# Kernel tuning notes

Measured on AMD Instinct MI355X. Metric: run time of the kernel, lower is better.

The kernel has to match this reference:

```python
import jax, jax.numpy as jnp
import numpy as np

B, S, E, H = 4, 2048, 1024, 16
D = E // H  # head_dim = 64
SCALE = D ** -0.5
NEG_INF = -1e9


def setup_inputs() -> dict:
    key = jax.random.key(0)
    ks = jax.random.split(key, 12)
    p = 1.0 / np.sqrt(E)  # nn.Linear default init scale
    inp = {
        'query': jax.random.normal(ks[0], (B, S, E), jnp.float32),
        'key': jax.random.normal(ks[1], (B, S, E), jnp.float32),
        'value': jax.random.normal(ks[2], (B, S, E), jnp.float32),
        'mask': jnp.ones((B, S, S), jnp.int32),
        'Wq': jax.random.uniform(ks[3], (E, E), jnp.float32, -p, p),
        'bq': jax.random.uniform(ks[4], (E,), jnp.float32, -p, p),
        'Wk': jax.random.uniform(ks[5], (E, E), jnp.float32, -p, p),
        'bk': jax.random.uniform(ks[6], (E,), jnp.float32, -p, p),
        'Wv': jax.random.uniform(ks[7], (E, E), jnp.float32, -p, p),
        'bv': jax.random.uniform(ks[8], (E,), jnp.float32, -p, p),
        'Wo': jax.random.uniform(ks[9], (E, E), jnp.float32, -p, p),
        'bo': jax.random.uniform(ks[10], (E,), jnp.float32, -p, p),
    }
    return inp


def _heads(x):
    # [B, S, E] -> [B, H, S, D]
    b, s, _ = x.shape
    return x.reshape(b, s, H, D).transpose(0, 2, 1, 3)


def reference(query, key, value, mask, Wq, bq, Wk, bk, Wv, bv, Wo, bo):
    # separate QKV projections (nn.Linear: x @ W.T + b)
    q = _heads(query @ Wq.T + bq) * SCALE  # query pre-scaled as in module
    k = _heads(key @ Wk.T + bk)
    v = _heads(value @ Wv.T + bv)
    # scaled dot-product attention with explicit score matrix
    scores = jnp.einsum('bhqd,bhkd->bhqk', q, k)  # [B, H, S, S]
    m = mask[:, None, :, :]  # broadcast over heads
    scores = jnp.where(m == 0, NEG_INF, scores)
    attn = jax.nn.softmax(scores, axis=-1)
    out = jnp.einsum('bhqk,bhkd->bhqd', attn, v)  # [B, H, S, D]
    out = out.transpose(0, 2, 1, 3).reshape(query.shape[0], -1, E)
    return out @ Wo.T + bo
```

## Files before the change

### kernel.cpp

```cpp
#include <hip/hip_runtime.h>


#define B_ 4
#define S_ 2048
#define E_ 1024
#define H_ 16
#define D_ 64

typedef __attribute__((ext_vector_type(4))) float f32x4;
typedef __attribute__((ext_vector_type(8))) short short8;
typedef __attribute__((ext_vector_type(4))) short short4v;
typedef __attribute__((ext_vector_type(8))) __bf16 bf16x8;
typedef __attribute__((ext_vector_type(4))) __bf16 bf16x4;
typedef unsigned short u16;
typedef unsigned int u32;

#define MFMA16(A, Bf, C) __builtin_amdgcn_mfma_f32_16x16x32_bf16((A), (Bf), (C), 0, 0, 0)

#define FMAXB2 12.0f

__device__ __forceinline__ f32x4 mfma_pv(short4v a, short4v b, f32x4 c) {
  return __builtin_amdgcn_mfma_f32_16x16x16bf16_1k(a, b, c, 0, 0, 0);
}

__device__ __forceinline__ u16 f2bf(float f) {
  u32 u = __float_as_uint(f);
  u += 0x7FFFu + ((u >> 16) & 1u);
  return (u16)(u >> 16);
}

__device__ __forceinline__ void async16(const void* g, void* l) {
  __builtin_amdgcn_global_load_lds((const __attribute__((address_space(1))) u32*)g,
                                   (__attribute__((address_space(3))) u32*)l, 16, 0, 0);
}

__device__ __forceinline__ short4v packp(float a, float b, float c, float d) {
  bf16x4 t;
  t[0] = (__bf16)a; t[1] = (__bf16)b; t[2] = (__bf16)c; t[3] = (__bf16)d;
  return __builtin_bit_cast(short4v, t);
}

__device__ __forceinline__ float exp2fast(float x) {
  return __builtin_amdgcn_exp2f(x);
}

__global__ __launch_bounds__(256) void cvt7_kernel(const float* __restrict__ a0,
                                                   const float* __restrict__ a1,
                                                   const float* __restrict__ a2,
                                                   const float* __restrict__ w0,
                                                   const float* __restrict__ w1,
                                                   const float* __restrict__ w2,
                                                   const float* __restrict__ w3,
                                                   u16* __restrict__ da0,
                                                   u16* __restrict__ da1,
                                                   u16* __restrict__ da2,
                                                   u16* __restrict__ dw0,
                                                   u16* __restrict__ dw1,
                                                   u16* __restrict__ dw2,
                                                   u16* __restrict__ dw3,
                                                   int n4a, int n4w) {
  int z = blockIdx.y;
  const float* src;
  u16* dst;
  int n4;
  switch (z) {
    case 0: src = a0; dst = da0; n4 = n4a; break;
    case 1: src = a1; dst = da1; n4 = n4a; break;
    case 2: src = a2; dst = da2; n4 = n4a; break;
    case 3: src = w0; dst = dw0; n4 = n4w; break;
    case 4: src = w1; dst = dw1; n4 = n4w; break;
    case 5: src = w2; dst = dw2; n4 = n4w; break;
    default: src = w3; dst = dw3; n4 = n4w; break;
  }
  int i = blockIdx.x * 256 + threadIdx.x;
  if (i >= n4) return;
  float4 v = ((const float4*)src)[i];
  short4v o;
  o[0] = (short)f2bf(v.x); o[1] = (short)f2bf(v.y);
  o[2] = (short)f2bf(v.z); o[3] = (short)f2bf(v.w);
  ((short4v*)dst)[i] = o;
}

__global__ __launch_bounds__(64) void mask_pack_kernel(const int* __restrict__ mask,
                                                       u32* __restrict__ mbits,
                                                       int* __restrict__ rowOK) {
  int row = blockIdx.x;
  int t = threadIdx.x;
  const int4* p = (const int4*)(mask + (size_t)row * S_ + t * 32);
  u32 bits = 0;
#pragma unroll
  for (int i = 0; i < 8; ++i) {
    int4 v = p[i];
    bits |= (v.x != 0 ? 1u : 0u) << (i * 4 + 0);
    bits |= (v.y != 0 ? 1u : 0u) << (i * 4 + 1);
    bits |= (v.z != 0 ? 1u : 0u) << (i * 4 + 2);
    bits |= (v.w != 0 ? 1u : 0u) << (i * 4 + 3);
  }
  mbits[(size_t)row * 64 + t] = bits;
  unsigned long long all1 = __ballot(bits == 0xFFFFFFFFu);
  if (t == 0) rowOK[row] = (all1 == 0xFFFFFFFFFFFFFFFFull) ? 1 : 0;
}

__device__ __forceinline__ void gemm_swizzle(int* m0, int* n0) {
  int s = blockIdx.y * 8 + blockIdx.x;
  int L = (s & 7) * 64 + (s >> 3);
  *m0 = (L >> 3) * 128;
  *n0 = (L & 7) * 128;
}

__device__ __forceinline__ void gemm_mainloop_128(const u16* __restrict__ A,
                                                  const u16* __restrict__ W,
                                                  int m0, int n0,
                                                  u16* As, u16* Bs,
                                                  f32x4 acc[4][4], int tid) {
  int w = tid >> 6, l = tid & 63, lo = l & 15, g = l >> 4;
  int wm = w >> 1, wn = w & 1;
  int srow = w * 32 + (l >> 3);
  int scol = ((l & 7) ^ (l >> 3)) * 8;
  const u16* ga0 = A + (size_t)(m0 + srow) * E_ + scol;
  const u16* gb0 = W + (size_t)(n0 + srow) * E_ + scol;
  char* la0 = (char*)As + w * 4096;
  char* lb0 = (char*)Bs + w * 4096;

  for (int k0 = 0; k0 < E_; k0 += 64) {
#pragma unroll
    for (int i = 0; i < 4; ++i) {
      async16(ga0 + (size_t)i * 8 * E_ + k0, la0 + i * 1024);
      async16(gb0 + (size_t)i * 8 * E_ + k0, lb0 + i * 1024);
    }
    __syncthreads();
#pragma unroll
    for (int kh = 0; kh < 2; ++kh) {
      bf16x8 af[4], bf[4];
#pragma unroll
      for (int mi = 0; mi < 4; ++mi) {
        int r = wm * 64 + mi * 16 + lo;
        af[mi] = *(const bf16x8*)((char*)As + r * 128 + (((kh * 4 + g) ^ (r & 7)) * 16));
      }
#pragma unroll
      for (int ni = 0; ni < 4; ++ni) {
        int r = wn * 64 + ni * 16 + lo;
        bf[ni] = *(const bf16x8*)((char*)Bs + r * 128 + (((kh * 4 + g) ^ (r & 7)) * 16));
      }
#pragma unroll
      for (int mi = 0; mi < 4; ++mi)
#pragma unroll
        for (int ni = 0; ni < 4; ++ni)
          acc[mi][ni] = MFMA16(af[mi], bf[ni], acc[mi][ni]);
    }
    __syncthreads();
  }
}

__global__ __launch_bounds__(256) void gemm_qkv_kernel(
    const u16* __restrict__ qin, const u16* __restrict__ kin, const u16* __restrict__ vin,
    const u16* __restrict__ wq, const u16* __restrict__ wk, const u16* __restrict__ wv,
    const float* __restrict__ bq, const float* __restrict__ bk, const float* __restrict__ bv,
    u16* __restrict__ Qo, u16* __restrict__ Ko, u16* __restrict__ Vo) {
  __shared__ u16 As[128 * 64];
  __shared__ u16 Bs[128 * 64];
  int z = blockIdx.z;
  const u16* A = z == 0 ? qin : (z == 1 ? kin : vin);
  const u16* W = z == 0 ? wq : (z == 1 ? wk : wv);
  const float* bias = z == 0 ? bq : (z == 1 ? bk : bv);
  u16* O = z == 0 ? Qo : (z == 1 ? Ko : Vo);
  float scale = z == 0 ? 0.125f * 1.44269504f : 1.0f;
  int m0, n0;
  gemm_swizzle(&m0, &n0);
  f32x4 acc[4][4];
#pragma unroll
  for (int mi = 0; mi < 4; ++mi)
#pragma unroll
    for (int ni = 0; ni < 4; ++ni) acc[mi][ni] = (f32x4){0.f, 0.f, 0.f, 0.f};
  int tid = threadIdx.x;
  gemm_mainloop_128(A, W, m0, n0, As, Bs, acc, tid);
  int w = tid >> 6, l = tid & 63, lo = l & 15, g = l >> 4;
  int wm = w >> 1, wn = w & 1;
#pragma unroll
  for (int mi = 0; mi < 4; ++mi)
#pragma unroll
    for (int ni = 0; ni < 4; ++ni) {
      int n = n0 + wn * 64 + ni * 16 + lo;
      int h = n >> 6, d = n & 63;
      float bb = bias[n];
      int mbase = m0 + wm * 64 + mi * 16 + g * 4;
      int b = mbase >> 11, s = mbase & 2047;
      if (z == 2) {
        short4v ov;
#pragma unroll
        for (int j = 0; j < 4; ++j) ov[j] = (short)f2bf(acc[mi][ni][j] + bb);
        *(short4v*)(O + (((size_t)(b * H_ + h)) * D_ + d) * S_ + s) = ov;
      } else {
#pragma unroll
        for (int j = 0; j < 4; ++j) {
          float val = (acc[mi][ni][j] + bb) * scale;
          O[(((size_t)(b * H_ + h)) * S_ + (s + j)) * D_ + d] = f2bf(val);
        }
      }
    }
}

__global__ __launch_bounds__(256) void gemm_out_kernel(const u16* __restrict__ A,
                                                       const u16* __restrict__ W,
                                                       const float* __restrict__ bias,
                                                       float* __restrict__ O) {
  __shared__ u16 As[128 * 64];
  __shared__ u16 Bs[128 * 64];
  int m0, n0;
  gemm_swizzle(&m0, &n0);
  f32x4 acc[4][4];
#pragma unroll
  for (int mi = 0; mi < 4; ++mi)
#pragma unroll
    for (int ni = 0; ni < 4; ++ni) acc[mi][ni] = (f32x4){0.f, 0.f, 0.f, 0.f};
  int tid = threadIdx.x;
  gemm_mainloop_128(A, W, m0, n0, As, Bs, acc, tid);
  int w = tid >> 6, l = tid & 63, lo = l & 15, g = l >> 4;
  int wm = w >> 1, wn = w & 1;
#pragma unroll
  for (int mi = 0; mi < 4; ++mi)
#pragma unroll
    for (int ni = 0; ni < 4; ++ni) {
      int n = n0 + wn * 64 + ni * 16 + lo;
      float bb = bias[n];
#pragma unroll
      for (int j = 0; j < 4; ++j) {
        int m = m0 + wm * 64 + mi * 16 + g * 4 + j;
        O[(size_t)m * E_ + n] = acc[mi][ni][j] + bb;
      }
    }
}

__global__ __launch_bounds__(256) void attn_kernel(const u16* __restrict__ Q,
                                                   const u16* __restrict__ K,
                                                   const u16* __restrict__ VT,
                                                   u16* __restrict__ AO,
                                                   const u32* __restrict__ mbits,
                                                   const int* __restrict__ rowOK) {
  __shared__ u16 Kt0[4096], Kt1[4096];
  __shared__ u16 Vt0[4096], Vt1[4096];
  __shared__ int s_ok;

  int tid = threadIdx.x;
  int w = tid >> 6, l = tid & 63, lo = l & 15, g = l >> 4;
  int flat = blockIdx.y * gridDim.x + blockIdx.x;
  int L = (flat & 7) * 128 + (flat >> 3);
  int bh = L >> 4;
  int b = bh >> 4, h = bh & 15;
  int q0 = (L & 15) * 128;

  if (tid == 0) s_ok = 1;
  __syncthreads();
  if (tid < 128 && rowOK[b * S_ + q0 + tid] == 0) s_ok = 0;
  __syncthreads();
  const bool use_mask = (s_ok == 0);

  const u16* Qb = Q + (size_t)bh * S_ * D_;
  const u16* Kb = K + (size_t)bh * S_ * D_;
  const u16* VTb = VT + (size_t)bh * D_ * S_;

  const u16* kg[2];
  const u16* vgb[2];
  int lbase[2];
#pragma unroll
  for (int r = 0; r < 2; ++r) {
    int kb = r * 4 + w;
    int tr = kb * 8 + (l >> 3);
    int dc = (l & 7) ^ (l >> 3);
    kg[r] = Kb + (size_t)tr * D_ + dc * 8;
    vgb[r] = VTb + (size_t)tr * S_ + dc * 8;
    lbase[r] = kb * 512;
  }
#pragma unroll
  for (int r = 0; r < 2; ++r) {
    async16(kg[r], &Kt0[lbase[r]]);
    async16(vgb[r], &Vt0[lbase[r]]);
  }

  int qrow = q0 + w * 32;
  bf16x8 qf[2][2];
#pragma unroll
  for (int qi = 0; qi < 2; ++qi)
#pragma unroll
    for (int kc = 0; kc < 2; ++kc)
      qf[qi][kc] = *(const bf16x8*)(Qb + (size_t)(qrow + qi * 16 + lo) * D_ + kc * 32 + g * 8);

  f32x4 ot[4][2];
  f32x4 lacc[2];
#pragma unroll
  for (int di = 0; di < 4; ++di)
#pragma unroll
    for (int qi = 0; qi < 2; ++qi) ot[di][qi] = (f32x4){0.f, 0.f, 0.f, 0.f};
  lacc[0] = (f32x4){0.f, 0.f, 0.f, 0.f};
  lacc[1] = (f32x4){0.f, 0.f, 0.f, 0.f};
  float m_run[2] = {-__builtin_inff(), -__builtin_inff()};
  const short4v onesv = {(short)0x3F80, (short)0x3F80, (short)0x3F80, (short)0x3F80};
  const f32x4 cinit = {-FMAXB2, -FMAXB2, -FMAXB2, -FMAXB2};

  auto tile_body = [&](const u16* KtC, const u16* VtC, u16* KtN, u16* VtN, int kk) {
    __syncthreads();
    if (kk + 64 < S_) {
#pragma unroll
      for (int r = 0; r < 2; ++r) {
        async16(kg[r] + (size_t)(kk + 64) * D_, &KtN[lbase[r]]);
        async16(vgb[r] + (kk + 64), &VtN[lbase[r]]);
      }
    }
    const char* Ktc = (const char*)KtC;
    const char* Vtc = (const char*)VtC;

    short4v pb[4][2];
    if (!use_mask) {
      __builtin_amdgcn_s_setprio(1);
#pragma unroll
      for (int ks = 0; ks < 4; ++ks) {
        int row = ks * 16 + lo;
        bf16x8 a0 = *(const bf16x8*)(Ktc + row * 128 + ((g * 16) ^ ((row & 7) << 4)));
        bf16x8 a1 = *(const bf16x8*)(Ktc + row * 128 + ((64 + g * 16) ^ ((row & 7) << 4)));
        f32x4 c0 = MFMA16(a0, qf[0][0], cinit);
        c0 = MFMA16(a1, qf[0][1], c0);
        f32x4 c1 = MFMA16(a0, qf[1][0], cinit);
        c1 = MFMA16(a1, qf[1][1], c1);
        pb[ks][0] = packp(exp2fast(c0[0]), exp2fast(c0[1]), exp2fast(c0[2]),
                          exp2fast(c0[3]));
        pb[ks][1] = packp(exp2fast(c1[0]), exp2fast(c1[1]), exp2fast(c1[2]),
                          exp2fast(c1[3]));
      }
      __builtin_amdgcn_s_setprio(0);
    } else {
      float tmx[2] = {-__builtin_inff(), -__builtin_inff()};
#pragma unroll
      for (int ks = 0; ks < 4; ++ks) {
        int row = ks * 16 + lo;
        bf16x8 a0 = *(const bf16x8*)(Ktc + row * 128 + ((g * 16) ^ ((row & 7) << 4)));
        bf16x8 a1 = *(const bf16x8*)(Ktc + row * 128 + ((64 + g * 16) ^ ((row & 7) << 4)));
#pragma unroll
        for (int qi = 0; qi < 2; ++qi) {
          f32x4 c = MFMA16(a0, qf[qi][0], cinit);
          c = MFMA16(a1, qf[qi][1], c);
          int q = qrow + qi * 16 + lo;
          u32 word = mbits[((size_t)(b * S_ + q)) * 64 + ((kk + ks * 16 + g * 4) >> 5)];
#pragma unroll
          for (int j = 0; j < 4; ++j) {
            int kkk = ks * 16 + g * 4 + j;
            if (!((word >> ((kk + kkk) & 31)) & 1u)) c[j] = -1e9f;
            tmx[qi] = fmaxf(tmx[qi], c[j]);
          }
        }
      }
#pragma unroll
      for (int qi = 0; qi < 2; ++qi) {
        float t = tmx[qi];
        t = fmaxf(t, __shfl_xor(t, 16, 64));
        t = fmaxf(t, __shfl_xor(t, 32, 64));
        float mnew = fmaxf(m_run[qi], t);
        float alpha = exp2fast(m_run[qi] - mnew);
        m_run[qi] = mnew;
#pragma unroll
        for (int di = 0; di < 4; ++di) ot[di][qi] *= alpha;
        lacc[qi] *= alpha;
      }
#pragma unroll
      for (int ks = 0; ks < 4; ++ks) {
        int row = ks * 16 + lo;
        bf16x8 a0 = *(const bf16x8*)(Ktc + row * 128 + ((g * 16) ^ ((row & 7) << 4)));
        bf16x8 a1 = *(const bf16x8*)(Ktc + row * 128 + ((64 + g * 16) ^ ((row & 7) << 4)));
#pragma unroll
        for (int qi = 0; qi < 2; ++qi) {
          f32x4 c = MFMA16(a0, qf[qi][0], cinit);
          c = MFMA16(a1, qf[qi][1], c);
          int q = qrow + qi * 16 + lo;
          u32 word = mbits[((size_t)(b * S_ + q)) * 64 + ((kk + ks * 16 + g * 4) >> 5)];
          float mm = m_run[qi];
#pragma unroll
          for (int j = 0; j < 4; ++j) {
            int kkk = ks * 16 + g * 4 + j;
            if (!((word >> ((kk + kkk) & 31)) & 1u)) c[j] = -1e9f;
            c[j] = exp2fast(c[j] - mm);
          }
          pb[ks][qi] = packp(c[0], c[1], c[2], c[3]);
        }
      }
    }

#pragma unroll
    for (int ks = 0; ks < 4; ++ks)
#pragma unroll
      for (int qi = 0; qi < 2; ++qi)
        lacc[qi] = mfma_pv(onesv, pb[ks][qi], lacc[qi]);

    short4v vaA[4], vaB[4];
#define LOADVA(arr, ksv)                                                              \
  _Pragma("unroll") for (int di = 0; di < 4; ++di) {                                  \
    int r = di * 16 + lo;                                                             \
    int chunk = (ksv)*2 + (g >> 1);                                                   \
    arr[di] = *(const short4v*)(Vtc + r * 128 + (((chunk * 16) ^ ((r & 7) << 4))) +   \
                                ((g & 1) * 8));                                       \
  }
#define MFMAKS(arr, ksv)                                                              \
  _Pragma("unroll") for (int qi = 0; qi < 2; ++qi) {                                  \
    _Pragma("unroll") for (int di = 0; di < 4; ++di)                                  \
        ot[di][qi] = mfma_pv(arr[di], pb[ksv][qi], ot[di][qi]);                       \
  }
    LOADVA(vaA, 0)
    LOADVA(vaB, 1)
    __builtin_amdgcn_s_setprio(1);
    MFMAKS(vaA, 0)
    LOADVA(vaA, 2)
    MFMAKS(vaB, 1)
    LOADVA(vaB, 3)
    MFMAKS(vaA, 2)
    MFMAKS(vaB, 3)
    __builtin_amdgcn_s_setprio(0);
#undef LOADVA
#undef MFMAKS
  };

  for (int k0 = 0; k0 < S_; k0 += 128) {
    tile_body(Kt0, Vt0, Kt1, Vt1, k0);
    tile_body(Kt1, Vt1, Kt0, Vt0, k0 + 64);
  }

#pragma unroll
  for (int qi = 0; qi < 2; ++qi) {
    float inv = 1.f / lacc[qi][0];
    int q = qrow + qi * 16 + lo;
#pragma unroll
    for (int di = 0; di < 4; ++di) {
      f32x4 o = ot[di][qi] * inv;
      short4v ov = packp(o[0], o[1], o[2], o[3]);
      *(short4v*)(AO + ((size_t)(b * S_ + q)) * E_ + h * 64 + di * 16 + g * 4) = ov;
    }
  }
}

extern "C" void kernel_launch(void* const* d_in, const int* in_sizes, int n_in,
                              void* d_out, int out_size, void* d_ws, size_t ws_size,
                              hipStream_t stream) {
  const float* query = (const float*)d_in[0];
  const float* key   = (const float*)d_in[1];
  const float* value = (const float*)d_in[2];
  const int*   mask  = (const int*)d_in[3];
  const float* Wq = (const float*)d_in[4];
  const float* bq = (const float*)d_in[5];
  const float* Wk = (const float*)d_in[6];
  const float* bk = (const float*)d_in[7];
  const float* Wv = (const float*)d_in[8];
  const float* bv = (const float*)d_in[9];
  const float* Wo = (const float*)d_in[10];
  const float* bo = (const float*)d_in[11];
  float* out = (float*)d_out;

  char* ws = (char*)d_ws;
  size_t off = 0;
  auto alloc = [&](size_t bytes) -> char* {
    char* p = ws + off;
    off += (bytes + 255) & ~(size_t)255;
    return p;
  };
  const size_t ACT = (size_t)8192 * 1024 * 2;
  const size_t WMT = (size_t)1024 * 1024 * 2;
  u16* qbf = (u16*)alloc(ACT);
  u16* kbf = (u16*)alloc(ACT);
  u16* vbf = (u16*)alloc(ACT);
  u16* wqb = (u16*)alloc(WMT);
  u16* wkb = (u16*)alloc(WMT);
  u16* wvb = (u16*)alloc(WMT);
  u16* wob = (u16*)alloc(WMT);
  u16* Qd = (u16*)alloc(ACT);
  u16* Kd = (u16*)alloc(ACT);
  u16* VTd = (u16*)alloc(ACT);
  u16* AO = (u16*)alloc(ACT);
  u32* mb = (u32*)alloc((size_t)B_ * S_ * 64 * 4);
  int* rOK = (int*)alloc((size_t)B_ * S_ * 4);
  (void)in_sizes; (void)n_in; (void)out_size; (void)ws_size;

  int n4a = B_ * S_ * E_ / 4;
  int n4w = E_ * E_ / 4;
  cvt7_kernel<<<dim3((n4a + 255) / 256, 7), 256, 0, stream>>>(
      query, key, value, Wq, Wk, Wv, Wo, qbf, kbf, vbf, wqb, wkb, wvb, wob, n4a, n4w);
  mask_pack_kernel<<<B_ * S_, 64, 0, stream>>>(mask, mb, rOK);
  gemm_qkv_kernel<<<dim3(8, 64, 3), 256, 0, stream>>>(
      qbf, kbf, vbf, wqb, wkb, wvb, bq, bk, bv, Qd, Kd, VTd);
  attn_kernel<<<dim3(16, 64), 256, 0, stream>>>(Qd, Kd, VTd, AO, mb, rOK);
  gemm_out_kernel<<<dim3(8, 64), 256, 0, stream>>>(AO, wob, bo, out);
}
```

Measured before the change: 234.7 us.

## Use 32x32x16 MFMA for PV, VALU row sums, fuse mask pack into convert

The PV product in attention switches from many 16x16x16 MFMAs to 32x32x16 MFMAs. The P fragments are rearranged across lane halves with ds_swizzle so they match the wider operand layout. The softmax denominator is now summed on the VALU with cross-lane shuffles instead of a ones-vector MFMA. The mask packing kernel is merged into the conversion kernel as an extra grid slice, saving one launch. This adds swizzle and select instructions per tile and changes the accumulator layout and output write pattern.

```diff
diff --git a/kernel.cpp b/kernel.cpp
--- a/kernel.cpp
+++ b/kernel.cpp
@@ -8,6 +8,7 @@
 #define D_ 64
 
 typedef __attribute__((ext_vector_type(4))) float f32x4;
+typedef __attribute__((ext_vector_type(16))) float f32x16;
 typedef __attribute__((ext_vector_type(8))) short short8;
 typedef __attribute__((ext_vector_type(4))) short short4v;
 typedef __attribute__((ext_vector_type(8))) __bf16 bf16x8;
@@ -16,12 +17,9 @@
 typedef unsigned int u32;
 
 #define MFMA16(A, Bf, C) __builtin_amdgcn_mfma_f32_16x16x32_bf16((A), (Bf), (C), 0, 0, 0)
+#define MFMA3216(A, Bf, C) __builtin_amdgcn_mfma_f32_32x32x16_bf16((A), (Bf), (C), 0, 0, 0)
 
 #define FMAXB2 12.0f
-
-__device__ __forceinline__ f32x4 mfma_pv(short4v a, short4v b, f32x4 c) {
-  return __builtin_amdgcn_mfma_f32_16x16x16bf16_1k(a, b, c, 0, 0, 0);
-}
 
 __device__ __forceinline__ u16 f2bf(float f) {
   u32 u = __float_as_uint(f);
@@ -44,7 +42,15 @@
   return __builtin_amdgcn_exp2f(x);
 }
 
-__global__ __launch_bounds__(256) void cvt7_kernel(const float* __restrict__ a0,
+__device__ __forceinline__ short4v swz16(short4v v) {
+  uint2 s = __builtin_bit_cast(uint2, v);
+  uint2 r;
+  r.x = (u32)__builtin_amdgcn_ds_swizzle((int)s.x, 0x401F);
+  r.y = (u32)__builtin_amdgcn_ds_swizzle((int)s.y, 0x401F);
+  return __builtin_bit_cast(short4v, r);
+}
+
+__global__ __launch_bounds__(256) void cvt8_kernel(const float* __restrict__ a0,
                                                    const float* __restrict__ a1,
                                                    const float* __restrict__ a2,
                                                    const float* __restrict__ w0,
@@ -58,8 +64,30 @@
                                                    u16* __restrict__ dw1,
                                                    u16* __restrict__ dw2,
                                                    u16* __restrict__ dw3,
+                                                   const int* __restrict__ mask,
+                                                   u32* __restrict__ mbits,
+                                                   int* __restrict__ rowOK,
                                                    int n4a, int n4w) {
   int z = blockIdx.y;
+  if (z == 7) {
+    if (blockIdx.x >= 2048) return;
+    int w = threadIdx.x >> 6, t = threadIdx.x & 63;
+    int row = blockIdx.x * 4 + w;
+    const int4* p = (const int4*)(mask + (size_t)row * S_ + t * 32);
+    u32 bits = 0;
+#pragma unroll
+    for (int i = 0; i < 8; ++i) {
+      int4 v = p[i];
+      bits |= (v.x != 0 ? 1u : 0u) << (i * 4 + 0);
+      bits |= (v.y != 0 ? 1u : 0u) << (i * 4 + 1);
+      bits |= (v.z != 0 ? 1u : 0u) << (i * 4 + 2);
+      bits |= (v.w != 0 ? 1u : 0u) << (i * 4 + 3);
+    }
+    mbits[(size_t)row * 64 + t] = bits;
+    unsigned long long all1 = __ballot(bits == 0xFFFFFFFFu);
+    if (t == 0) rowOK[row] = (all1 == 0xFFFFFFFFFFFFFFFFull) ? 1 : 0;
+    return;
+  }
   const float* src;
   u16* dst;
   int n4;
@@ -79,26 +107,6 @@
   o[0] = (short)f2bf(v.x); o[1] = (short)f2bf(v.y);
   o[2] = (short)f2bf(v.z); o[3] = (short)f2bf(v.w);
   ((short4v*)dst)[i] = o;
-}
-
-__global__ __launch_bounds__(64) void mask_pack_kernel(const int* __restrict__ mask,
-                                                       u32* __restrict__ mbits,
-                                                       int* __restrict__ rowOK) {
-  int row = blockIdx.x;
-  int t = threadIdx.x;
-  const int4* p = (const int4*)(mask + (size_t)row * S_ + t * 32);
-  u32 bits = 0;
-#pragma unroll
-  for (int i = 0; i < 8; ++i) {
-    int4 v = p[i];
-    bits |= (v.x != 0 ? 1u : 0u) << (i * 4 + 0);
-    bits |= (v.y != 0 ? 1u : 0u) << (i * 4 + 1);
-    bits |= (v.z != 0 ? 1u : 0u) << (i * 4 + 2);
-    bits |= (v.w != 0 ? 1u : 0u) << (i * 4 + 3);
-  }
-  mbits[(size_t)row * 64 + t] = bits;
-  unsigned long long all1 = __ballot(bits == 0xFFFFFFFFu);
-  if (t == 0) rowOK[row] = (all1 == 0xFFFFFFFFFFFFFFFFull) ? 1 : 0;
 }
 
 __device__ __forceinline__ void gemm_swizzle(int* m0, int* n0) {
@@ -243,6 +251,7 @@
 
   int tid = threadIdx.x;
   int w = tid >> 6, l = tid & 63, lo = l & 15, g = l >> 4;
+  int l4 = (l >> 4) & 1, l5 = l >> 5, q31 = l & 31;
   int flat = blockIdx.y * gridDim.x + blockIdx.x;
   int L = (flat & 7) * 128 + (flat >> 3);
   int bh = L >> 4;
@@ -285,16 +294,11 @@
     for (int kc = 0; kc < 2; ++kc)
       qf[qi][kc] = *(const bf16x8*)(Qb + (size_t)(qrow + qi * 16 + lo) * D_ + kc * 32 + g * 8);
 
-  f32x4 ot[4][2];
-  f32x4 lacc[2];
-#pragma unroll
-  for (int di = 0; di < 4; ++di)
-#pragma unroll
-    for (int qi = 0; qi < 2; ++qi) ot[di][qi] = (f32x4){0.f, 0.f, 0.f, 0.f};
-  lacc[0] = (f32x4){0.f, 0.f, 0.f, 0.f};
-  lacc[1] = (f32x4){0.f, 0.f, 0.f, 0.f};
+  f32x16 ot2[2];
+#pragma unroll
+  for (int i = 0; i < 16; ++i) { ot2[0][i] = 0.f; ot2[1][i] = 0.f; }
+  float lacc[2] = {0.f, 0.f};
   float m_run[2] = {-__builtin_inff(), -__builtin_inff()};
-  const short4v onesv = {(short)0x3F80, (short)0x3F80, (short)0x3F80, (short)0x3F80};
   const f32x4 cinit = {-FMAXB2, -FMAXB2, -FMAXB2, -FMAXB2};
 
   auto tile_body = [&](const u16* KtC, const u16* VtC, u16* KtN, u16* VtN, int kk) {
@@ -310,6 +314,7 @@
     const char* Vtc = (const char*)VtC;
 
     short4v pb[4][2];
+    float ps0 = 0.f, ps1 = 0.f;
     if (!use_mask) {
       __builtin_amdgcn_s_setprio(1);
 #pragma unroll
@@ -321,10 +326,14 @@
         c0 = MFMA16(a1, qf[0][1], c0);
         f32x4 c1 = MFMA16(a0, qf[1][0], cinit);
         c1 = MFMA16(a1, qf[1][1], c1);
-        pb[ks][0] = packp(exp2fast(c0[0]), exp2fast(c0[1]), exp2fast(c0[2]),
-                          exp2fast(c0[3]));
-        pb[ks][1] = packp(exp2fast(c1[0]), exp2fast(c1[1]), exp2fast(c1[2]),
-                          exp2fast(c1[3]));
+        float p00 = exp2fast(c0[0]), p01 = exp2fast(c0[1]);
+        float p02 = exp2fast(c0[2]), p03 = exp2fast(c0[3]);
+        float p10 = exp2fast(c1[0]), p11 = exp2fast(c1[1]);
+        float p12 = exp2fast(c1[2]), p13 = exp2fast(c1[3]);
+        ps0 += (p00 + p01) + (p02 + p03);
+        ps1 += (p10 + p11) + (p12 + p13);
+        pb[ks][0] = packp(p00, p01, p02, p03);
+        pb[ks][1] = packp(p10, p11, p12, p13);
       }
       __builtin_amdgcn_s_setprio(0);
     } else {
@@ -348,18 +357,20 @@
           }
         }
       }
+      float alpha[2];
 #pragma unroll
       for (int qi = 0; qi < 2; ++qi) {
         float t = tmx[qi];
         t = fmaxf(t, __shfl_xor(t, 16, 64));
         t = fmaxf(t, __shfl_xor(t, 32, 64));
         float mnew = fmaxf(m_run[qi], t);
-        float alpha = exp2fast(m_run[qi] - mnew);
+        alpha[qi] = exp2fast(m_run[qi] - mnew);
         m_run[qi] = mnew;
-#pragma unroll
-        for (int di = 0; di < 4; ++di) ot[di][qi] *= alpha;
-        lacc[qi] *= alpha;
-      }
+        lacc[qi] *= alpha[qi];
+      }
+      float al = l4 ? alpha[1] : alpha[0];
+#pragma unroll
+      for (int i = 0; i < 16; ++i) { ot2[0][i] *= al; ot2[1][i] *= al; }
 #pragma unroll
       for (int ks = 0; ks < 4; ++ks) {
         int row = ks * 16 + lo;
@@ -378,42 +389,43 @@
             if (!((word >> ((kk + kkk) & 31)) & 1u)) c[j] = -1e9f;
             c[j] = exp2fast(c[j] - mm);
           }
+          if (qi == 0) ps0 += (c[0] + c[1]) + (c[2] + c[3]);
+          else ps1 += (c[0] + c[1]) + (c[2] + c[3]);
           pb[ks][qi] = packp(c[0], c[1], c[2], c[3]);
         }
       }
     }
-
-#pragma unroll
-    for (int ks = 0; ks < 4; ++ks)
-#pragma unroll
-      for (int qi = 0; qi < 2; ++qi)
-        lacc[qi] = mfma_pv(onesv, pb[ks][qi], lacc[qi]);
-
-    short4v vaA[4], vaB[4];
-#define LOADVA(arr, ksv)                                                              \
-  _Pragma("unroll") for (int di = 0; di < 4; ++di) {                                  \
-    int r = di * 16 + lo;                                                             \
-    int chunk = (ksv)*2 + (g >> 1);                                                   \
-    arr[di] = *(const short4v*)(Vtc + r * 128 + (((chunk * 16) ^ ((r & 7) << 4))) +   \
-                                ((g & 1) * 8));                                       \
-  }
-#define MFMAKS(arr, ksv)                                                              \
-  _Pragma("unroll") for (int qi = 0; qi < 2; ++qi) {                                  \
-    _Pragma("unroll") for (int di = 0; di < 4; ++di)                                  \
-        ot[di][qi] = mfma_pv(arr[di], pb[ksv][qi], ot[di][qi]);                       \
-  }
-    LOADVA(vaA, 0)
-    LOADVA(vaB, 1)
+    ps0 += __shfl_xor(ps0, 16, 64); ps0 += __shfl_xor(ps0, 32, 64);
+    ps1 += __shfl_xor(ps1, 16, 64); ps1 += __shfl_xor(ps1, 32, 64);
+    lacc[0] += ps0;
+    lacc[1] += ps1;
+
+    bf16x8 frag[4];
+#pragma unroll
+    for (int t = 0; t < 4; ++t) {
+      short4v X = pb[t][0], Y = pb[t][1];
+      short4v send = l4 ? X : Y;
+      short4v recv = swz16(send);
+      short4v own = l4 ? Y : X;
+      short4v lo4 = l4 ? recv : own;
+      short4v hi4 = l4 ? own : recv;
+      short8 f;
+#pragma unroll
+      for (int j = 0; j < 4; ++j) { f[j] = lo4[j]; f[j + 4] = hi4[j]; }
+      frag[t] = __builtin_bit_cast(bf16x8, f);
+    }
+
     __builtin_amdgcn_s_setprio(1);
-    MFMAKS(vaA, 0)
-    LOADVA(vaA, 2)
-    MFMAKS(vaB, 1)
-    LOADVA(vaB, 3)
-    MFMAKS(vaA, 2)
-    MFMAKS(vaB, 3)
+#pragma unroll
+    for (int t = 0; t < 4; ++t) {
+#pragma unroll
+      for (int db = 0; db < 2; ++db) {
+        int r = db * 32 + q31;
+        bf16x8 va = *(const bf16x8*)(Vtc + r * 128 + (((2 * t + l5) * 16) ^ ((r & 7) << 4)));
+        ot2[db] = MFMA3216(va, frag[t], ot2[db]);
+      }
+    }
     __builtin_amdgcn_s_setprio(0);
-#undef LOADVA
-#undef MFMAKS
   };
 
   for (int k0 = 0; k0 < S_; k0 += 128) {
@@ -421,17 +433,17 @@
     tile_body(Kt1, Vt1, Kt0, Vt0, k0 + 64);
   }
 
-#pragma unroll
-  for (int qi = 0; qi < 2; ++qi) {
-    float inv = 1.f / lacc[qi][0];
-    int q = qrow + qi * 16 + lo;
-#pragma unroll
-    for (int di = 0; di < 4; ++di) {
-      f32x4 o = ot[di][qi] * inv;
-      short4v ov = packp(o[0], o[1], o[2], o[3]);
-      *(short4v*)(AO + ((size_t)(b * S_ + q)) * E_ + h * 64 + di * 16 + g * 4) = ov;
-    }
-  }
+  float inv = 1.f / (l4 ? lacc[1] : lacc[0]);
+  int q = qrow + q31;
+#pragma unroll
+  for (int db = 0; db < 2; ++db)
+#pragma unroll
+    for (int rg = 0; rg < 4; ++rg) {
+      int d = db * 32 + 8 * rg + 4 * l5;
+      short4v ov = packp(ot2[db][rg * 4 + 0] * inv, ot2[db][rg * 4 + 1] * inv,
+                         ot2[db][rg * 4 + 2] * inv, ot2[db][rg * 4 + 3] * inv);
+      *(short4v*)(AO + ((size_t)(b * S_ + q)) * E_ + h * 64 + d) = ov;
+    }
 }
 
 extern "C" void kernel_launch(void* const* d_in, const int* in_sizes, int n_in,
@@ -477,9 +489,9 @@
 
   int n4a = B_ * S_ * E_ / 4;
   int n4w = E_ * E_ / 4;
-  cvt7_kernel<<<dim3((n4a + 255) / 256, 7), 256, 0, stream>>>(
-      query, key, value, Wq, Wk, Wv, Wo, qbf, kbf, vbf, wqb, wkb, wvb, wob, n4a, n4w);
-  mask_pack_kernel<<<B_ * S_, 64, 0, stream>>>(mask, mb, rOK);
+  cvt8_kernel<<<dim3((n4a + 255) / 256, 8), 256, 0, stream>>>(
+      query, key, value, Wq, Wk, Wv, Wo, qbf, kbf, vbf, wqb, wkb, wvb, wob, mask, mb, rOK,
+      n4a, n4w);
   gemm_qkv_kernel<<<dim3(8, 64, 3), 256, 0, stream>>>(
       qbf, kbf, vbf, wqb, wkb, wvb, bq, bk, bv, Qd, Kd, VTd);
   attn_kernel<<<dim3(16, 64), 256, 0, stream>>>(Qd, Kd, VTd, AO, mb, rOK);
```

Measured after the change: 240.9 us. +2.6%, slower.
